# Optimization experiments

Measured on AMD Instinct MI355X. Metric: run time of the kernel, lower is better.

The kernel has to match this reference:

```python
import jax, jax.numpy as jnp
import numpy as np

N_NEURONS, RANK, N_CONV, LY, LX, BATCH = 8192, 1, 64, 36, 36, 256


def setup_inputs() -> dict:
    key = jax.random.key(0)
    k1, k2, k3, k4 = jax.random.split(key, 4)
    conv = jax.random.normal(k1, (BATCH, N_CONV, LY, LX), dtype=jnp.float32)
    Wc = 0.01 * jax.random.normal(k2, (N_NEURONS, RANK, N_CONV), dtype=jnp.float32)
    Wy = 0.01 * jax.random.normal(k3, (N_NEURONS, RANK, LY), dtype=jnp.float32)
    Wx = 0.01 * jax.random.normal(k4, (N_NEURONS, RANK, LX), dtype=jnp.float32)
    bias = jnp.zeros((N_NEURONS,), dtype=jnp.float32)
    return {"conv": conv, "Wc": Wc, "Wy": Wy, "Wx": Wx, "bias": bias}


def reference(conv, Wc, Wy, Wx, bias):
    # yx_separable, rank == 1 path of Readout.forward:
    #   pred = einsum('nrc,nry,icyx,nrx->in', Wc, Wy, conv, Wx)
    #   pred = elu(pred + bias)
    # Staged contraction: build per-neuron rank-1 spatial filter, contract
    # spatial dims first (small y*x=1296), then channels.
    Wyx = jnp.einsum('nry,nrx->nryx', Wy, Wx)              # [N, R, Ly, Lx]
    s = jnp.einsum('icyx,nryx->inrc', conv, Wyx)           # [B, N, R, C]
    pred = jnp.einsum('inrc,nrc->in', s, Wc)               # [B, N]
    return jax.nn.elu(pred + bias)
```

## Files before the change

kernel.cpp:

```cpp
#include <hip/hip_runtime.h>
#include <hip/hip_bf16.h>

#define NNEUR 8192
#define NCONV 64
#define LYC   36
#define LXC   36
#define BATCH 256
#define KRAW  1296
#define KPAD  1344
#define KITER 21
#define MROWS 16384
#define BM 256
#define BN 128
#define BK 64
#define ACH_PER_IT 2048
#define BCH_PER_IT 1024
#define A_TILE_H   (KITER * ACH_PER_IT * 8)
#define B_TILE_H   (KITER * BCH_PER_IT * 8)

typedef __attribute__((ext_vector_type(8))) _Float16 half8;
typedef __attribute__((ext_vector_type(4))) float f32x4;
typedef __attribute__((ext_vector_type(16))) float f32x16;

__device__ __forceinline__ void async_copy16(const void* g, void* l) {
  __builtin_amdgcn_global_load_lds(
      (const __attribute__((address_space(1))) void*)g,
      (__attribute__((address_space(3))) void*)l, 16, 0, 0);
}

__global__ __launch_bounds__(256) void prep_kernel(
    const float* __restrict__ conv, const float* __restrict__ Wy,
    const float* __restrict__ Wx, _Float16* __restrict__ A,
    _Float16* __restrict__ B) {
  const int t = threadIdx.x;
  const int bx = blockIdx.x;
  const int tile = blockIdx.y;
  const int slot = t & 7;
  half8 h;
  if (bx < 168) {
    const int it = bx >> 3, i = bx & 7;
    const int r = (t >> 3) + 32 * i;
    const int c = (slot - r) & 7;
    const int k0 = it * 64 + c * 8;
    const int grow = tile * BM + r;
    if (k0 < KRAW) {
      const float* s = conv + (size_t)grow * KRAW + k0;
#pragma unroll
      for (int e = 0; e < 8; e++) h[e] = (_Float16)s[e];
    } else {
#pragma unroll
      for (int e = 0; e < 8; e++) h[e] = (_Float16)0.f;
    }
    *(half8*)(A + (size_t)tile * A_TILE_H + ((size_t)bx * 256 + t) * 8) = h;
  } else {
    const int bx4 = bx - 168;
    const int it = bx4 >> 2, i = bx4 & 3;
    const int r = (t >> 3) + 32 * i;
    const int c = (slot - r) & 7;
    const int k0 = it * 64 + c * 8;
    const int n = tile * BN + r;
#pragma unroll
    for (int e = 0; e < 8; e++) {
      const int k = k0 + e;
      float v = 0.f;
      if (k < KRAW) {
        const int y = k / LXC;
        const int x = k - y * LXC;
        v = Wy[n * LYC + y] * Wx[n * LXC + x] * 256.f;
      }
      h[e] = (_Float16)v;
    }
    *(half8*)(B + (size_t)tile * B_TILE_H + ((size_t)bx4 * 256 + t) * 8) = h;
  }
}

__global__ __launch_bounds__(256, 3) void gemm_fused_kernel(
    const _Float16* __restrict__ A, const _Float16* __restrict__ B,
    const float* __restrict__ Wc, const float* __restrict__ bias,
    float* __restrict__ out) {
  __shared__ _Float16 As[BM * BK];
  __shared__ _Float16 Bs[BN * BK];

  const int bid = blockIdx.x;
  const int l = bid >> 3;
  const int ntile = (bid & 7) * 8 + (l & 7);
  const int mtile = l >> 3;
  const int tileN = ntile * BN;
  const int tileM = mtile * BM;

  const int t = threadIdx.x;
  const int lane = t & 63;
  const int wave = t >> 6;
  const int wm = wave >> 1, wn = wave & 1;
  const int r32 = lane & 31, hh = lane >> 5;

  f32x16 acc[4][2] = {};

  const _Float16* pA = A + (size_t)mtile * A_TILE_H;
  const _Float16* pB = B + (size_t)ntile * B_TILE_H;
  _Float16* lA = As + t * 8;
  _Float16* lB = Bs + t * 8;

  for (int it = 0; it < KITER; it++) {
    const _Float16* sA = pA + (size_t)it * (ACH_PER_IT * 8) + t * 8;
    const _Float16* sB = pB + (size_t)it * (BCH_PER_IT * 8) + t * 8;
#pragma unroll
    for (int i = 0; i < 8; i++) async_copy16(sA + i * 2048, lA + i * 2048);
#pragma unroll
    for (int i = 0; i < 4; i++) async_copy16(sB + i * 2048, lB + i * 2048);
    __syncthreads();

#pragma unroll
    for (int ks = 0; ks < 4; ks++) {
      const int cc = 2 * ks + hh;
      half8 bf[2];
#pragma unroll
      for (int nb = 0; nb < 2; nb++) {
        const int r = wn * 64 + nb * 32 + r32;
        bf[nb] = *(const half8*)(Bs + r * 64 + ((cc + r) & 7) * 8);
      }
#pragma unroll
      for (int mb = 0; mb < 4; mb++) {
        const int r = wm * 128 + mb * 32 + r32;
        const half8 af = *(const half8*)(As + r * 64 + ((cc + r) & 7) * 8);
#pragma unroll
        for (int nb = 0; nb < 2; nb++)
          acc[mb][nb] = __builtin_amdgcn_mfma_f32_32x32x16_f16(
              af, bf[nb], acc[mb][nb], 0, 0, 0);
      }
    }
    __syncthreads();
  }

  const int ibase = mtile * 4 + wm * 2;
  float v[2][2];
#pragma unroll
  for (int nb = 0; nb < 2; nb++) {
    const int n_g = tileN + wn * 64 + nb * 32 + r32;
    const float* wc = Wc + (size_t)n_g * NCONV;
    f32x4 w[2][4];
#pragma unroll
    for (int hf = 0; hf < 2; hf++)
#pragma unroll
      for (int g = 0; g < 4; g++)
        w[hf][g] = *(const f32x4*)(wc + hf * 32 + hh * 4 + g * 8);
#pragma unroll
    for (int img = 0; img < 2; img++) {
      float p = 0.f;
#pragma unroll
      for (int hf = 0; hf < 2; hf++)
#pragma unroll
        for (int g = 0; g < 4; g++)
#pragma unroll
          for (int q = 0; q < 4; q++)
            p += acc[img * 2 + hf][nb][g * 4 + q] * w[hf][g][q];
      p += __shfl_xor(p, 32);
      v[img][nb] = p;
    }
  }
  const int img = ibase + hh;
#pragma unroll
  for (int nb = 0; nb < 2; nb++) {
    const int n_out = tileN + wn * 64 + nb * 32 + r32;
    float z = v[hh][nb] * 0.00390625f + bias[n_out];
    z = z > 0.f ? z : (__expf(z) - 1.f);
    out[(size_t)img * NNEUR + n_out] = z;
  }
}

extern "C" void kernel_launch(void* const* d_in, const int* in_sizes, int n_in,
                              void* d_out, int out_size, void* d_ws,
                              size_t ws_size, hipStream_t stream) {
  const float* conv = (const float*)d_in[0];
  const float* Wc = (const float*)d_in[1];
  const float* Wy = (const float*)d_in[2];
  const float* Wx = (const float*)d_in[3];
  const float* bias = (const float*)d_in[4];
  float* out = (float*)d_out;

  _Float16* Abuf = (_Float16*)d_ws;
  _Float16* Bbuf = (_Float16*)((char*)d_ws + (size_t)MROWS * KPAD * 2);

  prep_kernel<<<dim3(252, 64), 256, 0, stream>>>(conv, Wy, Wx, Abuf, Bbuf);
  gemm_fused_kernel<<<4096, 256, 0, stream>>>(Abuf, Bbuf, Wc, bias, out);
}
```

Baseline: 481.1 us.

## Enlarge GEMM N-tile to 256 with 512-thread blocks and reflatten prep grid

Doubles the neuron tile from 128 to 256 and uses 8 waves per block in a 2x4 arrangement, so each A tile loaded into LDS feeds twice as many output columns. This halves the block count and the global and L2 traffic per FLOP for the activation operand. The prep kernel is rewritten to a flat 1D grid that emits the packed, swizzled layout for the new B tile size. The trade-off is more LDS per block (64 KB), occupancy capped at 2 blocks of 512 threads per CU, and a coarser tail.

```diff
diff --git a/kernel.cpp b/kernel.cpp
--- a/kernel.cpp
+++ b/kernel.cpp
@@ -11,12 +11,14 @@
 #define KITER 21
 #define MROWS 16384
 #define BM 256
-#define BN 128
+#define BN 256
 #define BK 64
-#define ACH_PER_IT 2048
-#define BCH_PER_IT 1024
-#define A_TILE_H   (KITER * ACH_PER_IT * 8)
-#define B_TILE_H   (KITER * BCH_PER_IT * 8)
+#define CH_PER_IT 2048
+#define TILE_H (KITER * CH_PER_IT * 8)
+#define A_NTILES 64
+#define B_NTILES 32
+#define A_PREP_BLOCKS 10752
+#define B_PREP_BLOCKS 5376
 
 typedef __attribute__((ext_vector_type(8))) _Float16 half8;
 typedef __attribute__((ext_vector_type(4))) float f32x4;
@@ -33,13 +35,13 @@
     const float* __restrict__ Wx, _Float16* __restrict__ A,
     _Float16* __restrict__ B) {
   const int t = threadIdx.x;
-  const int bx = blockIdx.x;
-  const int tile = blockIdx.y;
-  const int slot = t & 7;
   half8 h;
-  if (bx < 168) {
-    const int it = bx >> 3, i = bx & 7;
-    const int r = (t >> 3) + 32 * i;
+  if (blockIdx.x < A_PREP_BLOCKS) {
+    const int gid = blockIdx.x * 256 + t;
+    const int tile = gid / (KITER * CH_PER_IT);
+    const int rem = gid - tile * (KITER * CH_PER_IT);
+    const int it = rem >> 11, idx = rem & 2047;
+    const int r = idx >> 3, slot = idx & 7;
     const int c = (slot - r) & 7;
     const int k0 = it * 64 + c * 8;
     const int grow = tile * BM + r;
@@ -51,11 +53,13 @@
 #pragma unroll
       for (int e = 0; e < 8; e++) h[e] = (_Float16)0.f;
     }
-    *(half8*)(A + (size_t)tile * A_TILE_H + ((size_t)bx * 256 + t) * 8) = h;
+    *(half8*)(A + (size_t)tile * TILE_H + (size_t)rem * 8) = h;
   } else {
-    const int bx4 = bx - 168;
-    const int it = bx4 >> 2, i = bx4 & 3;
-    const int r = (t >> 3) + 32 * i;
+    const int gid = (blockIdx.x - A_PREP_BLOCKS) * 256 + t;
+    const int tile = gid / (KITER * CH_PER_IT);
+    const int rem = gid - tile * (KITER * CH_PER_IT);
+    const int it = rem >> 11, idx = rem & 2047;
+    const int r = idx >> 3, slot = idx & 7;
     const int c = (slot - r) & 7;
     const int k0 = it * 64 + c * 8;
     const int n = tile * BN + r;
@@ -70,11 +74,11 @@
       }
       h[e] = (_Float16)v;
     }
-    *(half8*)(B + (size_t)tile * B_TILE_H + ((size_t)bx4 * 256 + t) * 8) = h;
+    *(half8*)(B + (size_t)tile * TILE_H + (size_t)rem * 8) = h;
   }
 }
 
-__global__ __launch_bounds__(256, 3) void gemm_fused_kernel(
+__global__ __launch_bounds__(512, 2) void gemm_fused_kernel(
     const _Float16* __restrict__ A, const _Float16* __restrict__ B,
     const float* __restrict__ Wc, const float* __restrict__ bias,
     float* __restrict__ out) {
@@ -83,31 +87,29 @@
 
   const int bid = blockIdx.x;
   const int l = bid >> 3;
-  const int ntile = (bid & 7) * 8 + (l & 7);
-  const int mtile = l >> 3;
-  const int tileN = ntile * BN;
-  const int tileM = mtile * BM;
+  const int ntile = (bid & 7) * 4 + (l & 3);
+  const int mtile = l >> 2;
 
   const int t = threadIdx.x;
   const int lane = t & 63;
   const int wave = t >> 6;
-  const int wm = wave >> 1, wn = wave & 1;
+  const int wm = wave >> 2, wn = wave & 3;
   const int r32 = lane & 31, hh = lane >> 5;
 
   f32x16 acc[4][2] = {};
 
-  const _Float16* pA = A + (size_t)mtile * A_TILE_H;
-  const _Float16* pB = B + (size_t)ntile * B_TILE_H;
+  const _Float16* sA = A + (size_t)mtile * TILE_H + t * 8;
+  const _Float16* sB = B + (size_t)ntile * TILE_H + t * 8;
   _Float16* lA = As + t * 8;
   _Float16* lB = Bs + t * 8;
 
   for (int it = 0; it < KITER; it++) {
-    const _Float16* sA = pA + (size_t)it * (ACH_PER_IT * 8) + t * 8;
-    const _Float16* sB = pB + (size_t)it * (BCH_PER_IT * 8) + t * 8;
 #pragma unroll
-    for (int i = 0; i < 8; i++) async_copy16(sA + i * 2048, lA + i * 2048);
+    for (int i = 0; i < 4; i++) async_copy16(sA + i * 4096, lA + i * 4096);
 #pragma unroll
-    for (int i = 0; i < 4; i++) async_copy16(sB + i * 2048, lB + i * 2048);
+    for (int i = 0; i < 4; i++) async_copy16(sB + i * 4096, lB + i * 4096);
+    sA += CH_PER_IT * 8;
+    sB += CH_PER_IT * 8;
     __syncthreads();
 
 #pragma unroll
@@ -136,7 +138,7 @@
   float v[2][2];
 #pragma unroll
   for (int nb = 0; nb < 2; nb++) {
-    const int n_g = tileN + wn * 64 + nb * 32 + r32;
+    const int n_g = ntile * BN + wn * 64 + nb * 32 + r32;
     const float* wc = Wc + (size_t)n_g * NCONV;
     f32x4 w[2][4];
 #pragma unroll
@@ -161,7 +163,7 @@
   const int img = ibase + hh;
 #pragma unroll
   for (int nb = 0; nb < 2; nb++) {
-    const int n_out = tileN + wn * 64 + nb * 32 + r32;
+    const int n_out = ntile * BN + wn * 64 + nb * 32 + r32;
     float z = v[hh][nb] * 0.00390625f + bias[n_out];
     z = z > 0.f ? z : (__expf(z) - 1.f);
     out[(size_t)img * NNEUR + n_out] = z;
@@ -179,8 +181,10 @@
   float* out = (float*)d_out;
 
   _Float16* Abuf = (_Float16*)d_ws;
-  _Float16* Bbuf = (_Float16*)((char*)d_ws + (size_t)MROWS * KPAD * 2);
+  _Float16* Bbuf =
+      (_Float16*)((char*)d_ws + (size_t)A_NTILES * TILE_H * 2);
 
-  prep_kernel<<<dim3(252, 64), 256, 0, stream>>>(conv, Wy, Wx, Abuf, Bbuf);
-  gemm_fused_kernel<<<4096, 256, 0, stream>>>(Abuf, Bbuf, Wc, bias, out);
+  prep_kernel<<<A_PREP_BLOCKS + B_PREP_BLOCKS, 256, 0, stream>>>(conv, Wy, Wx,
+                                                                 Abuf, Bbuf);
+  gemm_fused_kernel<<<2048, 512, 0, stream>>>(Abuf, Bbuf, Wc, bias, out);
 }
```

After: 514.0 us. +6.8%, slower.
